# Performance work log

Measured on AMD Instinct MI355X. Metric: run time of the kernel, lower is better.

Reference implementation:

```python
import jax, jax.numpy as jnp
from jax import lax
import numpy as np

B, T, I, H, O = 8192, 2048, 1, 2, 1

def setup_inputs() -> dict:
    key = jax.random.key(0)
    ks = jax.random.split(key, 8)
    x = jax.random.normal(ks[0], (B, T, I), dtype=jnp.float32)
    lengths = jnp.maximum(1, jax.random.randint(ks[1], (B,), 0, T)).astype(jnp.int32)
    s_ih = 1.0 / np.sqrt(H)
    W_ih = jax.random.uniform(ks[2], (H, I), minval=-s_ih, maxval=s_ih, dtype=jnp.float32)
    W_hh = jax.random.uniform(ks[3], (H, H), minval=-s_ih, maxval=s_ih, dtype=jnp.float32)
    b_ih = jax.random.uniform(ks[4], (H,), minval=-s_ih, maxval=s_ih, dtype=jnp.float32)
    b_hh = jax.random.uniform(ks[5], (H,), minval=-s_ih, maxval=s_ih, dtype=jnp.float32)
    fc_w = jax.random.uniform(ks[6], (O, H), minval=-s_ih, maxval=s_ih, dtype=jnp.float32)
    fc_b = jax.random.uniform(ks[7], (O,), minval=-s_ih, maxval=s_ih, dtype=jnp.float32)
    return {"x": x, "lengths": lengths, "W_ih": W_ih, "W_hh": W_hh,
            "b_ih": b_ih, "b_hh": b_hh, "fc_w": fc_w, "fc_b": fc_b}

def reference(x, lengths, W_ih, W_hh, b_ih, b_hh, fc_w, fc_b):
    # x: [B, T, I]; tanh RNN, batch_first. pack_padded_sequence semantics:
    # hidden[-1][b] is the RNN state after lengths[b] steps of sequence b.
    Bn, Tn, _ = x.shape
    Hn = W_ih.shape[0]
    xs = jnp.moveaxis(x, 0, 1)                       # [T, B, I]
    valid = jnp.arange(Tn)[:, None] < lengths[None, :]  # [T, B]

    def step(h, inp):
        xt, v = inp                                  # xt [B,I], v [B]
        h_new = jnp.tanh(xt @ W_ih.T + b_ih + h @ W_hh.T + b_hh)
        h = jnp.where(v[:, None], h_new, h)          # freeze past each seq end
        return h, None

    h0 = jnp.zeros((Bn, Hn), dtype=x.dtype)
    h_final, _ = lax.scan(step, h0, (xs, valid))     # [B, H]
    # (The original computes a masked padded output but discards it.)
    return h_final @ fc_w.T + fc_b                   # [B, O]
```

## Files before the change

kernel.cpp:

```cpp
#include <hip/hip_runtime.h>
#include <cstdint>


#define T_LEN 2048

__device__ __forceinline__ float fast_exp2(float x) {
#if __has_builtin(__builtin_amdgcn_exp2f)
  return __builtin_amdgcn_exp2f(x);
#else
  return exp2f(x);
#endif
}

__device__ __forceinline__ float fast_rcp(float x) {
#if __has_builtin(__builtin_amdgcn_rcpf)
  return __builtin_amdgcn_rcpf(x);
#else
  return 1.0f / x;
#endif
}

__device__ __forceinline__ void rnn_step_r(float sg0, float sg1,
                                           float A00, float A01,
                                           float A10, float A11,
                                           float& r0, float& r1) {
  float u0 = fmaf(-A00, r0, fmaf(-A01, r1, sg0));
  float u1 = fmaf(-A10, r0, fmaf(-A11, r1, sg1));
  float e0 = fast_exp2(u0);
  float e1 = fast_exp2(u1);
  r0 = fast_rcp(e0 + 0.5f);
  r1 = fast_rcp(e1 + 0.5f);
}

__global__ __launch_bounds__(64) void rnn_scan(
    const float* __restrict__ x, const int* __restrict__ lengths,
    const float* __restrict__ wih, const float* __restrict__ whh,
    const float* __restrict__ bih, const float* __restrict__ bhh,
    const float* __restrict__ fcw, const float* __restrict__ fcb,
    float* __restrict__ out) {
  const int b = blockIdx.x * 64 + threadIdx.x;

  const float S = 2.885390081777926f;
  const float wa = whh[0], wb = whh[1], wc = whh[2], wd = whh[3];
  const float A00 = S * wa, A01 = S * wb;
  const float A10 = S * wc, A11 = S * wd;
  const float sw0 = S * wih[0];
  const float sw1 = S * wih[1];
  const float sc0 = fmaf(S, bih[0] + bhh[0], A00 + A01 - 1.0f);
  const float sc1 = fmaf(S, bih[1] + bhh[1], A10 + A11 - 1.0f);
  const float m0 = A00 + A01 - 1.0f;
  const float m1 = A10 + A11 - 1.0f;

  const float g11 = wa * wa + wc * wc;
  const float g22 = wb * wb + wd * wd;
  const float g12 = wa * wb + wc * wd;
  const float half_tr = 0.5f * (g11 + g22);
  const float half_df = 0.5f * (g11 - g22);
  const float s2 = half_tr + sqrtf(half_df * half_df + g12 * g12);
  const float sigma = sqrtf(s2) * 1.0002f;

  int K;
  if (sigma > 1e-4f && sigma < 0.999f) {
    K = (int)ceilf(-6.9078f / logf(sigma));
    if (K < 8) K = 8;
  } else if (!(sigma > 1e-4f)) {
    K = 8;
  } else {
    K = 1 << 20;
  }
  if (!(sigma == sigma)) K = 1 << 20;

  const int len = lengths[b];
  const float* __restrict__ xp = x + (size_t)b * T_LEN;

  float r0 = 1.0f, r1 = 1.0f;

  if (K <= 256) {
    const int Kp = (K + 15) & ~15;
    const int t0 = len - Kp;

    float xs[16];
#pragma unroll
    for (int i = 0; i < 16; ++i) {
      const int t = t0 + i;
      xs[i] = xp[min(max(t, 0), T_LEN - 1)];
    }
    for (int blk = 0; blk < Kp; blk += 16) {
      float xn[16];
#pragma unroll
      for (int i = 0; i < 16; ++i) {
        const int t = t0 + blk + 16 + i;
        xn[i] = xp[min(max(t, 0), T_LEN - 1)];
      }
#pragma unroll
      for (int i = 0; i < 16; ++i) {
        const int t = t0 + blk + i;
        const bool v = t >= 0;
        const float sg0 = v ? fmaf(sw0, xs[i], sc0) : m0;
        const float sg1 = v ? fmaf(sw1, xs[i], sc1) : m1;
        rnn_step_r(sg0, sg1, A00, A01, A10, A11, r0, r1);
      }
#pragma unroll
      for (int i = 0; i < 16; ++i) xs[i] = xn[i];
    }
  } else {
    const float4* __restrict__ xp4 = (const float4*)xp;
    const int ngroups = len >> 5;
    if (ngroups > 0) {
      float4 cur[8], nxt[8];
#pragma unroll
      for (int i = 0; i < 8; ++i) cur[i] = xp4[i];
      for (int g = 0; g < ngroups; ++g) {
        const int nb = min((g + 1) * 8, 504);
#pragma unroll
        for (int i = 0; i < 8; ++i) nxt[i] = xp4[nb + i];
#pragma unroll
        for (int i = 0; i < 8; ++i) {
          rnn_step_r(fmaf(sw0, cur[i].x, sc0), fmaf(sw1, cur[i].x, sc1),
                     A00, A01, A10, A11, r0, r1);
          rnn_step_r(fmaf(sw0, cur[i].y, sc0), fmaf(sw1, cur[i].y, sc1),
                     A00, A01, A10, A11, r0, r1);
          rnn_step_r(fmaf(sw0, cur[i].z, sc0), fmaf(sw1, cur[i].z, sc1),
                     A00, A01, A10, A11, r0, r1);
          rnn_step_r(fmaf(sw0, cur[i].w, sc0), fmaf(sw1, cur[i].w, sc1),
                     A00, A01, A10, A11, r0, r1);
        }
#pragma unroll
        for (int i = 0; i < 8; ++i) cur[i] = nxt[i];
      }
    }
    for (int t = ngroups << 5; t < len; ++t) {
      rnn_step_r(fmaf(sw0, xp[t], sc0), fmaf(sw1, xp[t], sc1),
                 A00, A01, A10, A11, r0, r1);
    }
  }

  const float fc0 = fcw[0], fc1 = fcw[1];
  const float csum = fc0 + fc1 + fcb[0];
  out[b] = fmaf(-fc0, r0, fmaf(-fc1, r1, csum));
}

extern "C" void kernel_launch(void* const* d_in, const int* in_sizes, int n_in,
                              void* d_out, int out_size, void* d_ws,
                              size_t ws_size, hipStream_t stream) {
  const float* x = (const float*)d_in[0];
  const int* lengths = (const int*)d_in[1];
  const float* wih = (const float*)d_in[2];
  const float* whh = (const float*)d_in[3];
  const float* bih = (const float*)d_in[4];
  const float* bhh = (const float*)d_in[5];
  const float* fcw = (const float*)d_in[6];
  const float* fcb = (const float*)d_in[7];
  float* out = (float*)d_out;

  const int B = 8192;
  rnn_scan<<<B / 64, 64, 0, stream>>>(x, lengths, wih, whh, bih, bhh, fcw,
                                      fcb, out);
}
```

Baseline: 101.5 us.

## Truncate non-contractive RNN scan using dual-trajectory convergence check with fallback

When the singular-value bound does not prove contraction, the kernel now runs only the last 384 steps. It runs them from two different initial states and accepts the result if the two trajectories agree within a small tolerance. Otherwise it falls back to the full sequential scan. This replaces up to the full sequence length of serial steps with a fixed window of doubled work, at the risk of accepting an approximation whenever agreement between the two probes does not imply agreement with the true zero-initialised state.

New measurement: 102.4 us. About the same (+0.9%).

```diff
diff --git a/kernel.cpp b/kernel.cpp
--- a/kernel.cpp
+++ b/kernel.cpp
@@ -3,6 +3,7 @@
 
 
 #define T_LEN 2048
+#define KE 384
 
 __device__ __forceinline__ float fast_exp2(float x) {
 #if __has_builtin(__builtin_amdgcn_exp2f)
@@ -104,35 +105,54 @@
       for (int i = 0; i < 16; ++i) xs[i] = xn[i];
     }
   } else {
-    const float4* __restrict__ xp4 = (const float4*)xp;
-    const int ngroups = len >> 5;
-    if (ngroups > 0) {
-      float4 cur[8], nxt[8];
+    const int t0 = len - KE;
+    float rA0 = 1.0f, rA1 = 1.0f;
+    float rB0 = 0.05f, rB1 = 1.95f;
+
+    float xs[16];
 #pragma unroll
-      for (int i = 0; i < 8; ++i) cur[i] = xp4[i];
-      for (int g = 0; g < ngroups; ++g) {
-        const int nb = min((g + 1) * 8, 504);
+    for (int i = 0; i < 16; ++i) {
+      const int t = t0 + i;
+      xs[i] = xp[min(max(t, 0), T_LEN - 1)];
+    }
+    for (int blk = 0; blk < KE; blk += 16) {
+      float xn[16];
 #pragma unroll
-        for (int i = 0; i < 8; ++i) nxt[i] = xp4[nb + i];
+      for (int i = 0; i < 16; ++i) {
+        const int t = t0 + blk + 16 + i;
+        xn[i] = xp[min(max(t, 0), T_LEN - 1)];
+      }
 #pragma unroll
-        for (int i = 0; i < 8; ++i) {
-          rnn_step_r(fmaf(sw0, cur[i].x, sc0), fmaf(sw1, cur[i].x, sc1),
-                     A00, A01, A10, A11, r0, r1);
-          rnn_step_r(fmaf(sw0, cur[i].y, sc0), fmaf(sw1, cur[i].y, sc1),
-                     A00, A01, A10, A11, r0, r1);
-          rnn_step_r(fmaf(sw0, cur[i].z, sc0), fmaf(sw1, cur[i].z, sc1),
-                     A00, A01, A10, A11, r0, r1);
-          rnn_step_r(fmaf(sw0, cur[i].w, sc0), fmaf(sw1, cur[i].w, sc1),
-                     A00, A01, A10, A11, r0, r1);
-        }
+      for (int i = 0; i < 16; ++i) {
+        const int t = t0 + blk + i;
+        const bool v = t >= 0;
+        const float sg0 = fmaf(sw0, xs[i], sc0);
+        const float sg1 = fmaf(sw1, xs[i], sc1);
+        float a0 = rA0, a1 = rA1;
+        rnn_step_r(sg0, sg1, A00, A01, A10, A11, a0, a1);
+        rA0 = v ? a0 : 1.0f;
+        rA1 = v ? a1 : 1.0f;
+        rnn_step_r(sg0, sg1, A00, A01, A10, A11, rB0, rB1);
+      }
 #pragma unroll
-        for (int i = 0; i < 8; ++i) cur[i] = nxt[i];
+      for (int i = 0; i < 16; ++i) xs[i] = xn[i];
+    }
+
+    const float diff = fmaxf(fabsf(rA0 - rB0), fabsf(rA1 - rB1));
+    const bool ok = (len <= KE)
+                    || (K <= KE)
+                    || (diff <= 4e-5f);
+
+    if (!ok) {
+      rA0 = 1.0f;
+      rA1 = 1.0f;
+      for (int t = 0; t < len; ++t) {
+        rnn_step_r(fmaf(sw0, xp[t], sc0), fmaf(sw1, xp[t], sc1),
+                   A00, A01, A10, A11, rA0, rA1);
       }
     }
-    for (int t = ngroups << 5; t < len; ++t) {
-      rnn_step_r(fmaf(sw0, xp[t], sc0), fmaf(sw1, xp[t], sc1),
-                 A00, A01, A10, A11, r0, r1);
-    }
+    r0 = rA0;
+    r1 = rA1;
   }
 
   const float fc0 = fcw[0], fc1 = fcw[1];
```
